# Optimization experiments

Measured on AMD Instinct MI355X. Metric: run time of the kernel, lower is better.

The kernel has to match this reference:

```python
import jax, jax.numpy as jnp
import numpy as np

B_, T_, DIN, H, DZ, DX = 64, 256, 128, 256, 8, 8


def setup_inputs() -> dict:
    key = jax.random.key(0)
    ks = jax.random.split(key, 13)
    p = lambda k, sh: jax.random.normal(k, sh, dtype=jnp.float32) * 0.05
    return {
        "y": jax.random.normal(ks[0], (B_, T_, DIN), dtype=jnp.float32),
        "W_ih": p(ks[1], (3 * H, DIN)), "W_hh": p(ks[2], (3 * H, H)),
        "b_ih": p(ks[3], (3 * H,)), "b_hh": p(ks[4], (3 * H,)),
        "W_mz": p(ks[5], (DZ, H)), "b_mz": p(ks[6], (DZ,)),
        "W_mx": p(ks[7], (DX, H)), "b_mx": p(ks[8], (DX,)),
        "W_pz": p(ks[9], (2 * DZ, H)), "b_pz": p(ks[10], (2 * DZ,)),
        "W_cx": p(ks[11], (DX * DX, H)), "b_cx": p(ks[12], (DX * DX,)),
    }


def _gru(y, W_ih, W_hh, b_ih, b_hh):
    # torch nn.GRU (single layer, unidirectional, batch_first)
    B, T, _ = y.shape
    Hh = W_hh.shape[1]
    x_proj = jnp.einsum('btd,gd->btg', y, W_ih) + b_ih  # [B,T,3H]

    def step(h, xp):
        hp = h @ W_hh.T + b_hh
        xr, xz, xn = jnp.split(xp, 3, axis=-1)
        hr, hz, hn = jnp.split(hp, 3, axis=-1)
        r = jax.nn.sigmoid(xr + hr)
        z = jax.nn.sigmoid(xz + hz)
        n = jnp.tanh(xn + r * hn)
        h_new = (1.0 - z) * n + z * h
        return h_new, h_new

    h0 = jnp.zeros((B, Hh), dtype=y.dtype)
    _, hs = jax.lax.scan(step, h0, jnp.swapaxes(x_proj, 0, 1))
    return jnp.swapaxes(hs, 0, 1)  # [B,T,H]


def _forward(y, W_ih, W_hh, b_ih, b_hh, W_mz, b_mz, W_mx, b_mx, W_pz, b_pz, W_cx, b_cx):
    enc = _gru(y, W_ih, W_hh, b_ih, b_hh)                       # [B,T,H]
    mean_z = enc @ W_mz.T + b_mz                                 # [B,T,DZ]
    mean_x = enc @ W_mx.T + b_mx                                 # [B,T,DX]
    bd_z = enc @ W_pz.T + b_pz                                   # [B,T,2*DZ]  (apply_softplus=False)

    # banded cov: per latent dim, upper-bidiagonal cholesky factor [B,T,T]
    diag = jnp.moveaxis(jax.nn.softplus(bd_z[..., :DZ]), -1, 0)  # [DZ,B,T]
    off = jnp.moveaxis(bd_z[:, :-1, DZ:], -1, 0)                 # [DZ,B,T-1]
    B, T = diag.shape[1], diag.shape[2]
    idx = jnp.arange(T)
    chol_z = (jnp.zeros((DZ, B, T, T), dtype=y.dtype)
              .at[:, :, idx, idx].set(diag)
              .at[:, :, idx[:-1], idx[1:]].set(off))             # [DZ,B,T,T]

    # anchor first two x-dims at t=0 (in-place mutation in torch)
    mean_x = mean_x.at[:, :, :2].add(-mean_x[:, 0:1, :2])
    mean_x_flat = mean_x.reshape(B * T, DX)

    cov_x = enc @ W_cx.T + b_cx                                  # [B,T,DX*DX]
    cov_x_flat = cov_x.reshape(B * T, DX, DX)
    return mean_z, chol_z, mean_x_flat, cov_x_flat


def reference(y, W_ih, W_hh, b_ih, b_hh, W_mz, b_mz, W_mx, b_mx, W_pz, b_pz, W_cx, b_cx):
    return _forward(y, W_ih, W_hh, b_ih, b_hh, W_mz, b_mz, W_mx, b_mx, W_pz, b_pz, W_cx, b_cx)
```

## Files before the change

### kernel.cpp

```cpp
#include <hip/hip_runtime.h>
#include <cstdint>
#include <cstddef>

#define B_   64
#define T_   256
#define DIN_ 128
#define H_   256
#define G3_  768

typedef _Float16 f16x8 __attribute__((ext_vector_type(8)));
typedef float    f32x4 __attribute__((ext_vector_type(4)));

#define MFMA(a, b, c) __builtin_amdgcn_mfma_f32_16x16x32_f16((a), (b), (c), 0, 0, 0)

__device__ __forceinline__ unsigned short f2h(float f) {
  _Float16 h = (_Float16)f;
  return __builtin_bit_cast(unsigned short, h);
}

__global__ __launch_bounds__(256) void prep_kernel(
    const float* __restrict__ W_ih, const float* __restrict__ W_hh,
    const float* __restrict__ W_mz, const float* __restrict__ W_mx,
    const float* __restrict__ W_pz, const float* __restrict__ W_cx,
    float* __restrict__ WT_ih, float* __restrict__ WheadT,
    unsigned* __restrict__ Wreg) {
  int i = blockIdx.x * 256 + threadIdx.x;
  if (i < 98304) {
    int k = i / 768, g = i % 768;
    WT_ih[i] = W_ih[g * 128 + k];
  } else if (i < 98304 + 24576) {
    int j = i - 98304;
    int c = j >> 8, k = j & 255;
    float v;
    if (c < 8)       v = W_mz[c * 256 + k];
    else if (c < 16) v = W_mx[(c - 8) * 256 + k];
    else if (c < 32) v = W_pz[(c - 16) * 256 + k];
    else             v = W_cx[(c - 32) * 256 + k];
    WheadT[j] = v;
  } else {
    int m = i - 122880;
    int c = m & 3, n = m >> 2;
    int tid = n & 511, j4 = n >> 9;
    int g   = j4 >> 4;
    int rem = j4 & 15;
    int uti = rem >> 3, kf = rem & 7;
    int wv = tid >> 6, l = tid & 63;
    int u = (2 * wv + uti) * 16 + (l & 15);
    int k = kf * 32 + ((l >> 4) << 3) + 2 * c;
    int row = g * 256 + u;
    unsigned short lo = f2h(W_hh[row * 256 + k]);
    unsigned short hi = f2h(W_hh[row * 256 + k + 1]);
    Wreg[m] = ((unsigned)hi << 16) | (unsigned)lo;
  }
}

__global__ __launch_bounds__(256) void xproj_kernel(
    const float* __restrict__ y, const float* __restrict__ WT_ih,
    const float* __restrict__ b_ih, const float* __restrict__ b_hh,
    float* __restrict__ xp) {
  __shared__ float ylds[64][132];
  int tid = threadIdx.x;
  int row0 = (blockIdx.x >> 1) * 64;
  int c0 = (blockIdx.x & 1) * 3;
  const float4* y4 = (const float4*)(y + (size_t)row0 * DIN_);
#pragma unroll
  for (int i = 0; i < 8; ++i) {
    int idx = i * 256 + tid;
    float4 v = y4[idx];
    int r = idx >> 5, c4 = (idx & 31) * 4;
    ylds[r][c4 + 0] = v.x; ylds[r][c4 + 1] = v.y;
    ylds[r][c4 + 2] = v.z; ylds[r][c4 + 3] = v.w;
  }
  __syncthreads();
  int tx = tid & 15, ty = tid >> 4;
  for (int c = c0; c < c0 + 3; ++c) {
    int col0 = c * 128 + tx * 8;
    float acc[4][8];
#pragma unroll
    for (int a = 0; a < 4; ++a)
#pragma unroll
      for (int b = 0; b < 8; ++b) acc[a][b] = 0.f;
#pragma unroll 4
    for (int k = 0; k < 128; ++k) {
      float4 w0 = *(const float4*)&WT_ih[k * 768 + col0];
      float4 w1 = *(const float4*)&WT_ih[k * 768 + col0 + 4];
      float a0 = ylds[ty * 4 + 0][k], a1 = ylds[ty * 4 + 1][k];
      float a2 = ylds[ty * 4 + 2][k], a3 = ylds[ty * 4 + 3][k];
      acc[0][0] += a0 * w0.x; acc[0][1] += a0 * w0.y; acc[0][2] += a0 * w0.z; acc[0][3] += a0 * w0.w;
      acc[0][4] += a0 * w1.x; acc[0][5] += a0 * w1.y; acc[0][6] += a0 * w1.z; acc[0][7] += a0 * w1.w;
      acc[1][0] += a1 * w0.x; acc[1][1] += a1 * w0.y; acc[1][2] += a1 * w0.z; acc[1][3] += a1 * w0.w;
      acc[1][4] += a1 * w1.x; acc[1][5] += a1 * w1.y; acc[1][6] += a1 * w1.z; acc[1][7] += a1 * w1.w;
      acc[2][0] += a2 * w0.x; acc[2][1] += a2 * w0.y; acc[2][2] += a2 * w0.z; acc[2][3] += a2 * w0.w;
      acc[2][4] += a2 * w1.x; acc[2][5] += a2 * w1.y; acc[2][6] += a2 * w1.z; acc[2][7] += a2 * w1.w;
      acc[3][0] += a3 * w0.x; acc[3][1] += a3 * w0.y; acc[3][2] += a3 * w0.z; acc[3][3] += a3 * w0.w;
      acc[3][4] += a3 * w1.x; acc[3][5] += a3 * w1.y; acc[3][6] += a3 * w1.z; acc[3][7] += a3 * w1.w;
    }
    float4 b0 = *(const float4*)&b_ih[col0];
    float4 b1 = *(const float4*)&b_ih[col0 + 4];
    if (c < 4) {
      float4 h0 = *(const float4*)&b_hh[col0];
      float4 h1 = *(const float4*)&b_hh[col0 + 4];
      b0.x += h0.x; b0.y += h0.y; b0.z += h0.z; b0.w += h0.w;
      b1.x += h1.x; b1.y += h1.y; b1.z += h1.z; b1.w += h1.w;
    }
#pragma unroll
    for (int a = 0; a < 4; ++a) {
      int row = row0 + ty * 4 + a;
      float4 o0, o1;
      o0.x = acc[a][0] + b0.x; o0.y = acc[a][1] + b0.y; o0.z = acc[a][2] + b0.z; o0.w = acc[a][3] + b0.w;
      o1.x = acc[a][4] + b1.x; o1.y = acc[a][5] + b1.y; o1.z = acc[a][6] + b1.z; o1.w = acc[a][7] + b1.w;
      *(float4*)&xp[(size_t)row * G3_ + col0] = o0;
      *(float4*)&xp[(size_t)row * G3_ + col0 + 4] = o1;
    }
  }
}

#define GRU_STEP(PAR, xr0, xz0, xn0, xr1, xz1, xn1,                            \
                 nxr0, nxz0, nxn0, nxr1, nxz1, nxn1)                           \
  {                                                                            \
    asm volatile("" ::: "memory");            \
    const int tc = t + PAR;                                                    \
    const float* xq = xpb + (size_t)(tc + 1) * G3_;          \
    nxr0 = xq[u0]; nxz0 = xq[256 + u0]; nxn0 = xq[512 + u0];                   \
    nxr1 = xq[u1]; nxz1 = xq[256 + u1]; nxn1 = xq[512 + u1];                   \
    uint4 hq0 = h4[PAR * 32 + g16];                                            \
    f16x8 hf0 = __builtin_bit_cast(f16x8, hq0);                                \
    f32x4 aR0 = MFMA(hf0, wf[0],  z4);  f32x4 aR1 = MFMA(hf0, wf[8],  z4);     \
    f32x4 aZ0 = MFMA(hf0, wf[16], z4);  f32x4 aZ1 = MFMA(hf0, wf[24], z4);     \
    f32x4 aN0 = MFMA(hf0, wf[32], z4);  f32x4 aN1 = MFMA(hf0, wf[40], z4);     \
    _Pragma("unroll")                                                          \
    for (int kf = 1; kf < 8; ++kf) {                                           \
      uint4 hq = h4[PAR * 32 + kf * 4 + g16];                                  \
      f16x8 hk = __builtin_bit_cast(f16x8, hq);                                \
      aR0 = MFMA(hk, wf[kf],      aR0); aR1 = MFMA(hk, wf[8 + kf],  aR1);      \
      aZ0 = MFMA(hk, wf[16 + kf], aZ0); aZ1 = MFMA(hk, wf[24 + kf], aZ1);      \
      aN0 = MFMA(hk, wf[32 + kf], aN0); aN1 = MFMA(hk, wf[40 + kf], aN1);      \
    }                                                                          \
             \
    float pr0 = aR0[0] + xr0, pr1 = aR1[0] + xr1;                              \
    float pz0 = aZ0[0] + xz0, pz1 = aZ1[0] + xz1;                              \
    float r0 = 1.f / (1.f + __expf(-pr0)), r1 = 1.f / (1.f + __expf(-pr1));    \
    float q0 = 1.f / (1.f + __expf(-pz0)), q1 = 1.f / (1.f + __expf(-pz1));    \
    float zh0 = q0 * hold0, zh1 = q1 * hold1;                                  \
    float om0 = 1.f - q0,   om1 = 1.f - q1;                                    \
    float pn0 = aN0[0] + bhn0, pn1 = aN1[0] + bhn1;                            \
    float a0 = xn0 + r0 * pn0, a1 = xn1 + r1 * pn1;                            \
    a0 = fminf(15.f, fmaxf(-15.f, a0)); a1 = fminf(15.f, fmaxf(-15.f, a1));    \
    float e0 = __expf(2.f * a0), e1 = __expf(2.f * a1);                        \
    float n0 = (e0 - 1.f) / (e0 + 1.f), n1 = (e1 - 1.f) / (e1 + 1.f);          \
    float h0n = om0 * n0 + zh0;                                                \
    float h1n = om1 * n1 + zh1;                                                \
    hold0 = h0n; hold1 = h1n;                 \
    if ((l >> 4) == 0) {                        \
      encb[tc * 256 + u0] = h0n;  encb[tc * 256 + u1] = h1n;                   \
      h16[PAR ^ 1][u0] = f2h(h0n); h16[PAR ^ 1][u1] = f2h(h1n);                \
    }                                                                          \
    __syncthreads();                                                           \
  }

__global__ __launch_bounds__(512) __attribute__((amdgpu_waves_per_eu(2, 2)))
void gru_kernel(
    const float* __restrict__ xp, const unsigned* Wreg,
    const float* __restrict__ b_hh, float* enc, float4* __restrict__ cholU) {
  int tid = threadIdx.x;
  int b = blockIdx.x;
  if (b >= 64) {
    float4 zz = {0.f, 0.f, 0.f, 0.f};
    int idx = (b - 64) * 512 + tid;
    for (; idx < 4194304; idx += 98304) cholU[idx] = zz;
    return;
  }
  int w = tid >> 6;
  int l = tid & 63;
  int g16 = l >> 4;
  int u0 = w * 32 + (l & 15);
  int u1 = u0 + 16;
  __shared__ alignas(16) unsigned short h16[2][256];

  f16x8 wf[48];
  const uint4* W4 = (const uint4*)Wreg;
#pragma unroll
  for (int fi = 0; fi < 48; ++fi) {
    uint4 q = W4[fi * 512 + tid];
    wf[fi] = __builtin_bit_cast(f16x8, q);
  }
  if (tid < 32) {
    uint4 z = {0u, 0u, 0u, 0u};
    ((uint4*)h16)[tid] = z;
  }
  const float* xpb = xp + (size_t)b * (T_ * G3_);
  float* encb = enc + (size_t)b * (T_ * H_);
  float bhn0 = b_hh[512 + u0], bhn1 = b_hh[512 + u1];
  float hold0 = 0.f, hold1 = 0.f;
  const f32x4 z4 = {0.f, 0.f, 0.f, 0.f};
  float xrA0 = xpb[u0], xzA0 = xpb[256 + u0], xnA0 = xpb[512 + u0];
  float xrA1 = xpb[u1], xzA1 = xpb[256 + u1], xnA1 = xpb[512 + u1];
  __syncthreads();
  const uint4* h4 = (const uint4*)h16;
  float xrB0, xzB0, xnB0, xrB1, xzB1, xnB1;
  for (int t = 0; t < T_; t += 2) {
    GRU_STEP(0, xrA0, xzA0, xnA0, xrA1, xzA1, xnA1,
                xrB0, xzB0, xnB0, xrB1, xzB1, xnB1)
    GRU_STEP(1, xrB0, xzB0, xnB0, xrB1, xzB1, xnB1,
                xrA0, xzA0, xnA0, xrA1, xzA1, xnA1)
  }
}

__global__ __launch_bounds__(384) void heads_kernel(
    const float* __restrict__ enc, const float* __restrict__ WheadT,
    const float* __restrict__ b_mz, const float* __restrict__ b_mx,
    const float* __restrict__ b_pz, const float* __restrict__ b_cx,
    float* __restrict__ out_meanz, float* __restrict__ out_meanx,
    float* __restrict__ out_covx, float* __restrict__ stage,
    float* __restrict__ chol, float* __restrict__ anchor,
    const float* __restrict__ W_mx) {
  int tid = threadIdx.x;
  if (blockIdx.x >= 512) {
    __shared__ float red[4];
    int bid = blockIdx.x - 512;
    int b = bid >> 1, d = bid & 1;
    if (tid < 256) {
      float v = enc[(size_t)b * (T_ * H_) + tid] * W_mx[d * 256 + tid];
#pragma unroll
      for (int off = 32; off >= 1; off >>= 1) v += __shfl_down(v, off, 64);
      if ((tid & 63) == 0) red[tid >> 6] = v;
    }
    __syncthreads();
    if (tid == 0)
      anchor[b * 2 + d] = b_mx[d] + ((red[0] + red[1]) + (red[2] + red[3]));
    return;
  }
  __shared__ float el[32 * 256];
  int row0 = blockIdx.x * 32;
  const float4* e4 = (const float4*)(enc + (size_t)row0 * 256);
  float4* el4 = (float4*)el;
#pragma unroll
  for (int i = 0; i < 6; ++i) {
    int idx = i * 384 + tid;
    if (idx < 2048) el4[idx] = e4[idx];
  }
  __syncthreads();
  int rg = tid / 96, c = tid - rg * 96;
  const float4* Wc = (const float4*)(WheadT + c * 256);
  float acc[8];
#pragma unroll
  for (int r = 0; r < 8; ++r) acc[r] = 0.f;
  for (int k4 = 0; k4 < 64; ++k4) {
    float4 w4 = Wc[k4];
#pragma unroll
    for (int r = 0; r < 8; ++r) {
      float4 ev = el4[(rg * 8 + r) * 64 + k4];
      acc[r] += w4.x * ev.x; acc[r] += w4.y * ev.y;
      acc[r] += w4.z * ev.z; acc[r] += w4.w * ev.w;
    }
  }
#pragma unroll
  for (int r = 0; r < 8; ++r) {
    int row = row0 + rg * 8 + r;
    float a_ = acc[r];
    if (c < 8) {
      out_meanz[(size_t)row * 8 + c] = a_ + b_mz[c];
    } else if (c < 16) {
      int d = c - 8;
      out_meanx[(size_t)row * 8 + d] = a_ + b_mx[d];
    } else if (c < 32) {
      int d = c - 16;
      float v = a_ + b_pz[d];
      if (d < 8)
        v = (v > 0.f) ? (v + log1pf(__expf(-v))) : log1pf(__expf(v));
      int bb = row >> 8, tt = row & 255;
      if (d < 4) {
        stage[(size_t)row * 16 + d] = v;
      } else if (d < 8) {
        chol[(((size_t)d * 64 + bb) * 256 + tt) * 256 + tt] = v;
      } else if (d < 12) {
        stage[(size_t)row * 16 + d] = v;
      } else {
        int dd = d - 8;
        if (tt < 255)
          chol[(((size_t)dd * 64 + bb) * 256 + tt) * 256 + tt + 1] = v;
      }
    } else {
      int d = c - 32;
      out_covx[(size_t)row * 64 + d] = a_ + b_cx[d];
    }
  }
}

__global__ __launch_bounds__(256) void chol_fin(
    const float* __restrict__ stage, float4* __restrict__ chol,
    const float* __restrict__ anchor, float* __restrict__ mean_x) {
  int i = blockIdx.x * 256 + threadIdx.x;
  int stride = gridDim.x * 256;
  for (; i < 4227072; i += stride) {
    if (i < 4194304) {
      int d = i >> 20;
      int bt = (i >> 6) & 16383;
      int t = bt & 255;
      int lane = i & 63;
      float vd = 0.f, vo = 0.f;
      if ((t >> 2) == lane)       vd = stage[bt * 16 + d];
      if (((t + 1) >> 2) == lane) vo = stage[bt * 16 + 8 + d];
      int te = t & 3, oe = (t + 1) & 3;
      float4 v;
      v.x = (te == 0 ? vd : 0.f) + (oe == 0 ? vo : 0.f);
      v.y = (te == 1 ? vd : 0.f) + (oe == 1 ? vo : 0.f);
      v.z = (te == 2 ? vd : 0.f) + (oe == 2 ? vo : 0.f);
      v.w = (te == 3 ? vd : 0.f) + (oe == 3 ? vo : 0.f);
      chol[i] = v;
    } else {
      int j2 = i - 4194304;
      int row = j2 >> 1, d = j2 & 1;
      mean_x[(size_t)row * 8 + d] -= anchor[(row >> 8) * 2 + d];
    }
  }
}

extern "C" void kernel_launch(void* const* d_in, const int* in_sizes, int n_in,
                              void* d_out, int out_size, void* d_ws, size_t ws_size,
                              hipStream_t stream) {
  const float* y    = (const float*)d_in[0];
  const float* W_ih = (const float*)d_in[1];
  const float* W_hh = (const float*)d_in[2];
  const float* b_ih = (const float*)d_in[3];
  const float* b_hh = (const float*)d_in[4];
  const float* W_mz = (const float*)d_in[5];
  const float* b_mz = (const float*)d_in[6];
  const float* W_mx = (const float*)d_in[7];
  const float* b_mx = (const float*)d_in[8];
  const float* W_pz = (const float*)d_in[9];
  const float* b_pz = (const float*)d_in[10];
  const float* W_cx = (const float*)d_in[11];
  const float* b_cx = (const float*)d_in[12];

  float* out    = (float*)d_out;
  float* mean_z = out;
  float* chol   = out + 131072;
  float* mean_x = out + 33685504;
  float* cov_x  = out + 33816576;

  float* ws      = (float*)d_ws;
  float* WT_ih   = ws;
  float* WheadT  = ws + 98304;
  unsigned* Wreg = (unsigned*)(ws + 122880);
  float* anchor  = ws + 221184;
  float* stage   = ws + 221312;

  float* xp  = chol;
  float* enc = chol + 12582912;

  prep_kernel<<<864, 256, 0, stream>>>(W_ih, W_hh, W_mz, W_mx, W_pz, W_cx,
                                       WT_ih, WheadT, Wreg);
  xproj_kernel<<<512, 256, 0, stream>>>(y, WT_ih, b_ih, b_hh, xp);
  gru_kernel<<<256, 512, 0, stream>>>(xp, Wreg, b_hh, enc,
                                      ((float4*)chol) + 4194304);
  heads_kernel<<<640, 384, 0, stream>>>(enc, WheadT, b_mz, b_mx, b_pz, b_cx,
                                        mean_z, mean_x, cov_x, stage,
                                        chol, anchor, W_mx);
  chol_fin<<<4096, 256, 0, stream>>>(stage, (float4*)chol, anchor, mean_x);
}
```

Measured before the change: 557.9 us.

## Split GRU recurrence across 16 waves with one hidden unit per lane

The GRU kernel moves from 512 to 1024 threads per block, so each wave owns 16 hidden units instead of 32. Each lane now holds 24 weight fragments instead of 48 and issues 24 MFMAs per step instead of 48, which shortens the serial per-step critical path. The software prefetch of the next step's input projection is removed and loads happen inside the step, which may expose latency. The zero-fill blocks are reduced to 96, and prep_kernel's register-packing layout is rewritten to match.

```diff
diff --git a/kernel.cpp b/kernel.cpp
--- a/kernel.cpp
+++ b/kernel.cpp
@@ -39,14 +39,12 @@
     WheadT[j] = v;
   } else {
     int m = i - 122880;
-    int c = m & 3, n = m >> 2;
-    int tid = n & 511, j4 = n >> 9;
-    int g   = j4 >> 4;
-    int rem = j4 & 15;
-    int uti = rem >> 3, kf = rem & 7;
+    int d = m & 3, n = m >> 2;
+    int tid = n & 1023, fi = n >> 10;
+    int g  = fi >> 3, kf = fi & 7;
     int wv = tid >> 6, l = tid & 63;
-    int u = (2 * wv + uti) * 16 + (l & 15);
-    int k = kf * 32 + ((l >> 4) << 3) + 2 * c;
+    int u = wv * 16 + (l & 15);
+    int k = kf * 32 + ((l >> 4) << 3) + 2 * d;
     int row = g * 256 + u;
     unsigned short lo = f2h(W_hh[row * 256 + k]);
     unsigned short hi = f2h(W_hh[row * 256 + k + 1]);
@@ -115,74 +113,30 @@
   }
 }
 
-#define GRU_STEP(PAR, xr0, xz0, xn0, xr1, xz1, xn1,                            \
-                 nxr0, nxz0, nxn0, nxr1, nxz1, nxn1)                           \
-  {                                                                            \
-    asm volatile("" ::: "memory");            \
-    const int tc = t + PAR;                                                    \
-    const float* xq = xpb + (size_t)(tc + 1) * G3_;          \
-    nxr0 = xq[u0]; nxz0 = xq[256 + u0]; nxn0 = xq[512 + u0];                   \
-    nxr1 = xq[u1]; nxz1 = xq[256 + u1]; nxn1 = xq[512 + u1];                   \
-    uint4 hq0 = h4[PAR * 32 + g16];                                            \
-    f16x8 hf0 = __builtin_bit_cast(f16x8, hq0);                                \
-    f32x4 aR0 = MFMA(hf0, wf[0],  z4);  f32x4 aR1 = MFMA(hf0, wf[8],  z4);     \
-    f32x4 aZ0 = MFMA(hf0, wf[16], z4);  f32x4 aZ1 = MFMA(hf0, wf[24], z4);     \
-    f32x4 aN0 = MFMA(hf0, wf[32], z4);  f32x4 aN1 = MFMA(hf0, wf[40], z4);     \
-    _Pragma("unroll")                                                          \
-    for (int kf = 1; kf < 8; ++kf) {                                           \
-      uint4 hq = h4[PAR * 32 + kf * 4 + g16];                                  \
-      f16x8 hk = __builtin_bit_cast(f16x8, hq);                                \
-      aR0 = MFMA(hk, wf[kf],      aR0); aR1 = MFMA(hk, wf[8 + kf],  aR1);      \
-      aZ0 = MFMA(hk, wf[16 + kf], aZ0); aZ1 = MFMA(hk, wf[24 + kf], aZ1);      \
-      aN0 = MFMA(hk, wf[32 + kf], aN0); aN1 = MFMA(hk, wf[40 + kf], aN1);      \
-    }                                                                          \
-             \
-    float pr0 = aR0[0] + xr0, pr1 = aR1[0] + xr1;                              \
-    float pz0 = aZ0[0] + xz0, pz1 = aZ1[0] + xz1;                              \
-    float r0 = 1.f / (1.f + __expf(-pr0)), r1 = 1.f / (1.f + __expf(-pr1));    \
-    float q0 = 1.f / (1.f + __expf(-pz0)), q1 = 1.f / (1.f + __expf(-pz1));    \
-    float zh0 = q0 * hold0, zh1 = q1 * hold1;                                  \
-    float om0 = 1.f - q0,   om1 = 1.f - q1;                                    \
-    float pn0 = aN0[0] + bhn0, pn1 = aN1[0] + bhn1;                            \
-    float a0 = xn0 + r0 * pn0, a1 = xn1 + r1 * pn1;                            \
-    a0 = fminf(15.f, fmaxf(-15.f, a0)); a1 = fminf(15.f, fmaxf(-15.f, a1));    \
-    float e0 = __expf(2.f * a0), e1 = __expf(2.f * a1);                        \
-    float n0 = (e0 - 1.f) / (e0 + 1.f), n1 = (e1 - 1.f) / (e1 + 1.f);          \
-    float h0n = om0 * n0 + zh0;                                                \
-    float h1n = om1 * n1 + zh1;                                                \
-    hold0 = h0n; hold1 = h1n;                 \
-    if ((l >> 4) == 0) {                        \
-      encb[tc * 256 + u0] = h0n;  encb[tc * 256 + u1] = h1n;                   \
-      h16[PAR ^ 1][u0] = f2h(h0n); h16[PAR ^ 1][u1] = f2h(h1n);                \
-    }                                                                          \
-    __syncthreads();                                                           \
-  }
-
-__global__ __launch_bounds__(512) __attribute__((amdgpu_waves_per_eu(2, 2)))
-void gru_kernel(
-    const float* __restrict__ xp, const unsigned* Wreg,
+__global__ __launch_bounds__(1024) void gru_kernel(
+    const float* __restrict__ xp, const unsigned* __restrict__ Wreg,
     const float* __restrict__ b_hh, float* enc, float4* __restrict__ cholU) {
   int tid = threadIdx.x;
   int b = blockIdx.x;
   if (b >= 64) {
     float4 zz = {0.f, 0.f, 0.f, 0.f};
-    int idx = (b - 64) * 512 + tid;
+    int idx = (b - 64) * 1024 + tid;
     for (; idx < 4194304; idx += 98304) cholU[idx] = zz;
     return;
   }
   int w = tid >> 6;
   int l = tid & 63;
   int g16 = l >> 4;
-  int u0 = w * 32 + (l & 15);
-  int u1 = u0 + 16;
+  int u = w * 16 + (l & 15);
   __shared__ alignas(16) unsigned short h16[2][256];
 
-  f16x8 wf[48];
+  f16x8 wfR[8], wfZ[8], wfN[8];
   const uint4* W4 = (const uint4*)Wreg;
 #pragma unroll
-  for (int fi = 0; fi < 48; ++fi) {
-    uint4 q = W4[fi * 512 + tid];
-    wf[fi] = __builtin_bit_cast(f16x8, q);
+  for (int kf = 0; kf < 8; ++kf) {
+    wfR[kf] = __builtin_bit_cast(f16x8, W4[(0 * 8 + kf) * 1024 + tid]);
+    wfZ[kf] = __builtin_bit_cast(f16x8, W4[(1 * 8 + kf) * 1024 + tid]);
+    wfN[kf] = __builtin_bit_cast(f16x8, W4[(2 * 8 + kf) * 1024 + tid]);
   }
   if (tid < 32) {
     uint4 z = {0u, 0u, 0u, 0u};
@@ -190,19 +144,48 @@
   }
   const float* xpb = xp + (size_t)b * (T_ * G3_);
   float* encb = enc + (size_t)b * (T_ * H_);
-  float bhn0 = b_hh[512 + u0], bhn1 = b_hh[512 + u1];
-  float hold0 = 0.f, hold1 = 0.f;
+  float bhn = b_hh[512 + u];
+  float hold = 0.f;
   const f32x4 z4 = {0.f, 0.f, 0.f, 0.f};
-  float xrA0 = xpb[u0], xzA0 = xpb[256 + u0], xnA0 = xpb[512 + u0];
-  float xrA1 = xpb[u1], xzA1 = xpb[256 + u1], xnA1 = xpb[512 + u1];
   __syncthreads();
   const uint4* h4 = (const uint4*)h16;
-  float xrB0, xzB0, xnB0, xrB1, xzB1, xnB1;
-  for (int t = 0; t < T_; t += 2) {
-    GRU_STEP(0, xrA0, xzA0, xnA0, xrA1, xzA1, xnA1,
-                xrB0, xzB0, xnB0, xrB1, xzB1, xnB1)
-    GRU_STEP(1, xrB0, xzB0, xnB0, xrB1, xzB1, xnB1,
-                xrA0, xzA0, xnA0, xrA1, xzA1, xnA1)
+  for (int t = 0; t < T_; ++t) {
+    asm volatile("" ::: "memory");
+    const float* xq = xpb + (size_t)t * G3_;
+    float xr = xq[u], xz = xq[256 + u], xn = xq[512 + u];
+    int cur = t & 1;
+    f32x4 aR, aZ, aN;
+    {
+      uint4 hq = h4[cur * 32 + g16];
+      f16x8 hk = __builtin_bit_cast(f16x8, hq);
+      aR = MFMA(hk, wfR[0], z4);
+      aZ = MFMA(hk, wfZ[0], z4);
+      aN = MFMA(hk, wfN[0], z4);
+    }
+#pragma unroll
+    for (int kf = 1; kf < 8; ++kf) {
+      uint4 hq = h4[cur * 32 + kf * 4 + g16];
+      f16x8 hk = __builtin_bit_cast(f16x8, hq);
+      aR = MFMA(hk, wfR[kf], aR);
+      aZ = MFMA(hk, wfZ[kf], aZ);
+      aN = MFMA(hk, wfN[kf], aN);
+    }
+    float pr = aR[0] + xr, pz = aZ[0] + xz;
+    float r_ = 1.f / (1.f + __expf(-pr));
+    float q_ = 1.f / (1.f + __expf(-pz));
+    float zh = q_ * hold, om = 1.f - q_;
+    float pn = aN[0] + bhn;
+    float a = xn + r_ * pn;
+    a = fminf(15.f, fmaxf(-15.f, a));
+    float e = __expf(2.f * a);
+    float n = (e - 1.f) / (e + 1.f);
+    float hn = om * n + zh;
+    hold = hn;
+    if (g16 == 0) {
+      encb[t * 256 + u] = hn;
+      h16[cur ^ 1][u] = f2h(hn);
+    }
+    __syncthreads();
   }
 }
 
@@ -352,8 +335,8 @@
   prep_kernel<<<864, 256, 0, stream>>>(W_ih, W_hh, W_mz, W_mx, W_pz, W_cx,
                                        WT_ih, WheadT, Wreg);
   xproj_kernel<<<512, 256, 0, stream>>>(y, WT_ih, b_ih, b_hh, xp);
-  gru_kernel<<<256, 512, 0, stream>>>(xp, Wreg, b_hh, enc,
-                                      ((float4*)chol) + 4194304);
+  gru_kernel<<<160, 1024, 0, stream>>>(xp, Wreg, b_hh, enc,
+                                       ((float4*)chol) + 4194304);
   heads_kernel<<<640, 384, 0, stream>>>(enc, WheadT, b_mz, b_mx, b_pz, b_cx,
                                         mean_z, mean_x, cov_x, stage,
                                         chol, anchor, W_mx);
```

New measurement: 546.0 us. 2.1% less time.
